# Performance work log

Hardware: AMD Instinct MI355X
Metric: run time of the kernel (lower is better)

Reference implementation:

```python
import jax, jax.numpy as jnp
import numpy as np
from jax import lax

A_RATIOS = (0.5, 1.0, 2.0)
A_SCALES = (8, 16, 32)
FEAT_STRIDE = 16
BASE_SIZE = 16
PRE_NMS = 6000     # n_test_pre_nms
POST_NMS = 300     # n_test_post_nms
NMS_THRESH = 0.7
MIN_SIZE = 16.0
SCALE = 1.0        # forward(scale=1.0) default
NEG = -1e10


def _anchor_base():
    # standard generate_anchor_base: centered at (8,8), ratios x scales
    py = px = BASE_SIZE / 2.0
    rows = []
    for r in A_RATIOS:
        for s in A_SCALES:
            h = BASE_SIZE * s * np.sqrt(r)
            w = BASE_SIZE * s * np.sqrt(1.0 / r)
            rows.append([py - h / 2.0, px - w / 2.0, py + h / 2.0, px + w / 2.0])
    return np.asarray(rows, np.float32)  # (A, 4)


def _all_anchors(height, width):
    base = jnp.asarray(_anchor_base())                                  # (A, 4)
    sy = (jnp.arange(height) * FEAT_STRIDE).astype(jnp.float32)
    sx = (jnp.arange(width) * FEAT_STRIDE).astype(jnp.float32)
    gy, gx = jnp.meshgrid(sy, sx, indexing='ij')
    shift = jnp.stack([gy.ravel(), gx.ravel(), gy.ravel(), gx.ravel()], axis=1)  # (K, 4)
    anch = base[None, :, :] + shift[:, None, :]                         # (K, A, 4)
    return anch.reshape(-1, 4)                                          # (K*A, 4)


def _conv(x, w, b, pad):
    y = lax.conv_general_dilated(x, w, (1, 1), [(pad, pad), (pad, pad)],
                                 dimension_numbers=('NCHW', 'OIHW', 'NCHW'))
    return y + b[None, :, None, None]


def _loc2bbox(anchors, locs):
    h = anchors[:, 2] - anchors[:, 0]
    w = anchors[:, 3] - anchors[:, 1]
    cy = anchors[:, 0] + 0.5 * h
    cx = anchors[:, 1] + 0.5 * w
    dy, dx, dh, dw = locs[:, 0], locs[:, 1], locs[:, 2], locs[:, 3]
    ncy = dy * h + cy
    ncx = dx * w + cx
    nh = jnp.exp(dh) * h
    nw = jnp.exp(dw) * w
    return jnp.stack([ncy - 0.5 * nh, ncx - 0.5 * nw,
                      ncy + 0.5 * nh, ncx + 0.5 * nw], axis=1)


def _iou_one_vs_all(box, boxes):
    ty = jnp.maximum(box[0], boxes[:, 0])
    tx = jnp.maximum(box[1], boxes[:, 1])
    by = jnp.minimum(box[2], boxes[:, 2])
    bx = jnp.minimum(box[3], boxes[:, 3])
    inter = jnp.maximum(by - ty, 0.0) * jnp.maximum(bx - tx, 0.0)
    a1 = (box[2] - box[0]) * (box[3] - box[1])
    a2 = (boxes[:, 2] - boxes[:, 0]) * (boxes[:, 3] - boxes[:, 1])
    return inter / (a1 + a2 - inter + 1e-9)


def _nms(boxes, scores):
    # greedy NMS with fixed POST_NMS output; invalid slots are zero boxes
    def step(s, _):
        i = jnp.argmax(s)
        valid = s[i] > NEG / 2
        ious = _iou_one_vs_all(boxes[i], boxes)
        s = jnp.where(ious > NMS_THRESH, NEG, s)  # suppresses self (iou=1)
        return s, (i, valid)
    _, (idx, valid) = lax.scan(step, scores, None, length=POST_NMS)
    return boxes[idx] * valid[:, None].astype(boxes.dtype)  # (POST_NMS, 4)


def _proposals(anchors, locs, fg, img_h, img_w):
    boxes = _loc2bbox(anchors, locs)
    boxes = jnp.stack([jnp.clip(boxes[:, 0], 0.0, img_h),
                       jnp.clip(boxes[:, 1], 0.0, img_w),
                       jnp.clip(boxes[:, 2], 0.0, img_h),
                       jnp.clip(boxes[:, 3], 0.0, img_w)], axis=1)
    hs = boxes[:, 2] - boxes[:, 0]
    ws = boxes[:, 3] - boxes[:, 1]
    ok = (hs >= MIN_SIZE * SCALE) & (ws >= MIN_SIZE * SCALE)
    sc = jnp.where(ok, fg, NEG)
    top_sc, idx = lax.top_k(sc, PRE_NMS)
    return _nms(boxes[idx], top_sc)


def reference(base_feat, W_conv1, b_conv1, W_score, b_score, W_loc, b_loc, img_h, img_w):
    N, _, H, W = base_feat.shape
    A = 9
    mid = jax.nn.relu(_conv(base_feat, W_conv1, b_conv1, 1))            # (N,512,H,W)
    rpn_locs = _conv(mid, W_loc, b_loc, 0).transpose(0, 2, 3, 1).reshape(N, H * W * A, 4)
    raw = _conv(mid, W_score, b_score, 0).transpose(0, 2, 3, 1)          # (N,H,W,2A)
    rpn_scores = raw.reshape(N, H * W * A, 2)
    fg = jax.nn.softmax(raw.reshape(N, H, W, A, 2), axis=-1)[..., 1].reshape(N, -1)
    anchors = _all_anchors(H, W)                                         # (H*W*A,4)
    ih, iw = float(img_h), float(img_w)
    prop = jax.vmap(lambda l, f: _proposals(anchors, l, f, ih, iw))(rpn_locs, fg)
    rois = prop.reshape(N * POST_NMS, 4)
    roi_indices = jnp.repeat(jnp.arange(N, dtype=jnp.int32), POST_NMS)
    return rpn_locs, rpn_scores, rois, roi_indices, anchors


def setup_inputs() -> dict:
    key = jax.random.key(0)
    k0, k1, k2, k3 = jax.random.split(key, 4)
    N, C, H, W = 4, 512, 64, 64
    nA = 9
    return {
        'base_feat': jax.random.normal(k0, (N, C, H, W), jnp.float32),
        'W_conv1': 0.01 * jax.random.normal(k1, (512, 512, 3, 3), jnp.float32),
        'b_conv1': jnp.zeros((512,), jnp.float32),
        'W_score': 0.01 * jax.random.normal(k2, (2 * nA, 512, 1, 1), jnp.float32),
        'b_score': jnp.zeros((2 * nA,), jnp.float32),
        'W_loc': 0.01 * jax.random.normal(k3, (4 * nA, 512, 1, 1), jnp.float32),
        'b_loc': jnp.zeros((4 * nA,), jnp.float32),
        'img_h': 1024,
        'img_w': 1024,
    }
```

## Files before the change

kernel.cpp:

```cpp
#include <hip/hip_runtime.h>
#include <math.h>

#define HH 64
#define WW 64
#define NIMG 4
#define CIN 512
#define AA 9
#define HWA (HH*WW*AA)
#define PRE_NMS 6000
#define POST_NMS 300
#define NEGV (-1e10f)
#define NEGK 0xD01502F9u
#define NWORD 94

#define OFF1 589824
#define OFF2 884736
#define OFF3 889536
#define OFF4 890736

typedef unsigned int u32;
typedef unsigned long long u64;
typedef _Float16 f16;
typedef _Float16 half8 __attribute__((ext_vector_type(8)));
typedef float f32x4 __attribute__((ext_vector_type(4)));

__device__ __forceinline__ void gload_lds16(const void* g, void* l)
{
    __builtin_amdgcn_global_load_lds((const __attribute__((address_space(1))) void*)g,
                                     (__attribute__((address_space(3))) void*)l,
                                     16, 0, 0);
}

__global__ __launch_bounds__(256) void k_prep_x(const float* __restrict__ x,
                                                f16* __restrict__ xh,
                                                f16* __restrict__ xl)
{
    __shared__ float tile[64][65];
    int ci0 = blockIdx.x * 64, y = blockIdx.y, n = blockIdx.z;
    int t = threadIdx.x;
    #pragma unroll
    for (int l = 0; l < 16; ++l) {
        int idx = l * 256 + t;
        int cc = idx >> 6, xc = idx & 63;
        tile[cc][xc] = x[((size_t)(n * CIN + ci0 + cc) * HH + y) * WW + xc];
    }
    __syncthreads();
    #pragma unroll
    for (int l = 0; l < 16; ++l) {
        int idx = l * 256 + t;
        int xc = idx >> 6, cc = idx & 63;
        float v = tile[cc][xc];
        f16 hi = (f16)v;
        f16 lo = (f16)(v - (float)hi);
        size_t o = ((size_t)(n * 64 + y) * 64 + xc) * 512 + ci0 + cc;
        xh[o] = hi; xl[o] = lo;
    }
}

__global__ __launch_bounds__(256) void k_prep_w(const float* __restrict__ W1,
                                                f16* __restrict__ wh,
                                                f16* __restrict__ wl)
{
    int idx = blockIdx.x * 256 + threadIdx.x;
    int co = idx >> 9, ci = idx & 511;
    #pragma unroll
    for (int tap = 0; tap < 9; ++tap) {
        float v = W1[(size_t)idx * 9 + tap];
        f16 hi = (f16)v;
        f16 lo = (f16)(v - (float)hi);
        size_t o = ((size_t)tap * 512 + co) * 512 + ci;
        wh[o] = hi; wl[o] = lo;
    }
}

__global__ __launch_bounds__(256, 4) void k_conv_mfma(const f16* __restrict__ xh,
                                                      const f16* __restrict__ xl,
                                                      const f16* __restrict__ wh,
                                                      const f16* __restrict__ wl,
                                                      const float* __restrict__ bias,
                                                      float* __restrict__ mid)
{
    __shared__ f16 sX[2][4][64][32];
    const int t = threadIdx.x;
    const int yb = blockIdx.x, co0 = blockIdx.y * 64, n = blockIdx.z;
    const int y0 = yb * 2;
    const int wv = t >> 6, lane = t & 63;
    const int q = lane >> 4, li = lane & 15;
    const int mh = wv & 1;
    const int xhp = wv >> 1;

    if (yb == 0 || yb == 31) {
        int rowu = (yb == 0) ? 0 : 3072;
        u32* p = (u32*)&sX[0][0][0][0];
        #pragma unroll
        for (int l = 0; l < 8; ++l) {
            int idx = l * 256 + t;
            int plane = idx >> 10, r = idx & 1023;
            p[plane * 4096 + rowu + r] = 0;
        }
    }

    f32x4 acc[2][2][2];
    #pragma unroll
    for (int mt = 0; mt < 2; ++mt)
        #pragma unroll
        for (int xn = 0; xn < 2; ++xn)
            #pragma unroll
            for (int yy = 0; yy < 2; ++yy)
                acc[mt][xn][yy] = (f32x4){0.f, 0.f, 0.f, 0.f};

    auto prefetch = [&](int ci0) {
        #pragma unroll
        for (int m = 0; m < 8; ++m) {
            int k2 = wv * 8 + m;
            int plane = k2 >> 4;
            int row = (k2 >> 2) & 3;
            int gy = y0 - 1 + row;
            if ((unsigned)gy < 64u) {
                int col = ((k2 & 3) << 4) + (lane >> 2);
                int s = lane & 3;
                const f16* src = (plane ? xl : xh) +
                    (((size_t)(n * 64 + gy) * 64 + col) * 512 + ci0 + s * 8);
                f16* dst = &sX[0][0][0][0] + (size_t)k2 * 512 + lane * 8;
                gload_lds16(src, dst);
            }
        }
    };

    half8 wa[2][2], wn[2][2];
    auto loadW = [&](half8 w[2][2], int ci0, int tap) {
        #pragma unroll
        for (int mt = 0; mt < 2; ++mt) {
            size_t base = ((size_t)(tap * 512) + co0 + mh * 32 + mt * 16 + li) * 512 + ci0 + q * 8;
            w[0][mt] = *(const half8*)(wh + base);
            w[1][mt] = *(const half8*)(wl + base);
        }
    };

    prefetch(0);
    loadW(wa, 0, 0);

    const half8 zero8 = {(f16)0, (f16)0, (f16)0, (f16)0, (f16)0, (f16)0, (f16)0, (f16)0};

    for (int chunk = 0; chunk < 16; ++chunk) {
        const int ci0 = chunk * 32;
        __syncthreads();

        #pragma unroll
        for (int tap = 0; tap < 9; ++tap) {
            if (tap < 8) loadW(wn, ci0, tap + 1);
            const int ky = tap / 3, kx = tap - ky * 3;

            half8 B[2][2][2];
            #pragma unroll
            for (int xn = 0; xn < 2; ++xn) {
                int xc = xhp * 32 + xn * 16 + li;
                int colr = xc + kx - 1;
                bool oob = (colr < 0) || (colr > 63);
                int colc = oob ? 0 : colr;
                #pragma unroll
                for (int yy = 0; yy < 2; ++yy) {
                    int row = yy + ky;
                    const f16* ph = &sX[0][row][colc][q * 8];
                    half8 vh = *(const half8*)ph;
                    half8 vl = *(const half8*)(ph + 8192);
                    if (oob) { vh = zero8; vl = zero8; }
                    B[0][xn][yy] = vh; B[1][xn][yy] = vl;
                }
            }
            #pragma unroll
            for (int mt = 0; mt < 2; ++mt)
                #pragma unroll
                for (int xn = 0; xn < 2; ++xn)
                    #pragma unroll
                    for (int yy = 0; yy < 2; ++yy)
                        acc[mt][xn][yy] = __builtin_amdgcn_mfma_f32_16x16x32_f16(wa[0][mt], B[0][xn][yy], acc[mt][xn][yy], 0, 0, 0);
            #pragma unroll
            for (int mt = 0; mt < 2; ++mt)
                #pragma unroll
                for (int xn = 0; xn < 2; ++xn)
                    #pragma unroll
                    for (int yy = 0; yy < 2; ++yy)
                        acc[mt][xn][yy] = __builtin_amdgcn_mfma_f32_16x16x32_f16(wa[0][mt], B[1][xn][yy], acc[mt][xn][yy], 0, 0, 0);
            #pragma unroll
            for (int mt = 0; mt < 2; ++mt)
                #pragma unroll
                for (int xn = 0; xn < 2; ++xn)
                    #pragma unroll
                    for (int yy = 0; yy < 2; ++yy)
                        acc[mt][xn][yy] = __builtin_amdgcn_mfma_f32_16x16x32_f16(wa[1][mt], B[0][xn][yy], acc[mt][xn][yy], 0, 0, 0);

            if (tap < 8) {
                #pragma unroll
                for (int pl = 0; pl < 2; ++pl)
                    #pragma unroll
                    for (int mt = 0; mt < 2; ++mt) wa[pl][mt] = wn[pl][mt];
            }
        }

        if (chunk + 1 < 16) {
            __syncthreads();
            prefetch(ci0 + 32);
            loadW(wa, ci0 + 32, 0);
        }
    }

    #pragma unroll
    for (int mt = 0; mt < 2; ++mt) {
        #pragma unroll
        for (int r = 0; r < 4; ++r) {
            int co = co0 + mh * 32 + mt * 16 + q * 4 + r;
            float bv = bias[co];
            #pragma unroll
            for (int xn = 0; xn < 2; ++xn) {
                int xc = xhp * 32 + xn * 16 + li;
                #pragma unroll
                for (int yy = 0; yy < 2; ++yy) {
                    float v = acc[mt][xn][yy][r] + bv;
                    mid[((size_t)(n * 512 + co) * HH + y0 + yy) * WW + xc] = v > 0.f ? v : 0.f;
                }
            }
        }
    }
}

__global__ __launch_bounds__(256) void k_htrans(const float* __restrict__ Ws,
                                                const float* __restrict__ Wl,
                                                float* __restrict__ Wt2)
{
    int i = blockIdx.x * 256 + threadIdx.x;
    if (i >= 512 * 64) return;
    int ci = i >> 6, co = i & 63;
    float v = 0.f;
    if (co < 18) v = Ws[co * 512 + ci];
    else if (co < 54) v = Wl[(co - 18) * 512 + ci];
    Wt2[i] = v;
}

__global__ __launch_bounds__(256) void k_hgemm(const float* __restrict__ mid,
                                               const float* __restrict__ Wt2,
                                               float* __restrict__ sraw)
{
    __shared__ float sM[32][64];
    __shared__ float sW2[32][64];
    const int t = threadIdx.x;
    const int px0 = blockIdx.x * 64, n = blockIdx.y;
    const int tx = t & 15, ty = t >> 4;

    float acc[4][4];
    #pragma unroll
    for (int c = 0; c < 4; ++c)
        #pragma unroll
        for (int j = 0; j < 4; ++j) acc[c][j] = 0.f;

    for (int ci0 = 0; ci0 < 512; ci0 += 32) {
        __syncthreads();
        #pragma unroll
        for (int l = 0; l < 8; ++l) {
            int i = l * 256 + t;
            int ci = i >> 6, px = i & 63;
            sM[ci][px] = mid[((size_t)n * 512 + ci0 + ci) * 4096 + px0 + px];
            sW2[ci][px] = Wt2[(size_t)(ci0 + ci) * 64 + px];
        }
        __syncthreads();
        #pragma unroll
        for (int ci = 0; ci < 32; ++ci) {
            float mv[4], wv[4];
            #pragma unroll
            for (int j = 0; j < 4; ++j) mv[j] = sM[ci][tx * 4 + j];
            #pragma unroll
            for (int c = 0; c < 4; ++c) wv[c] = sW2[ci][ty * 4 + c];
            #pragma unroll
            for (int c = 0; c < 4; ++c)
                #pragma unroll
                for (int j = 0; j < 4; ++j) acc[c][j] += wv[c] * mv[j];
        }
    }
    #pragma unroll
    for (int c = 0; c < 4; ++c) {
        float4 v = make_float4(acc[c][0], acc[c][1], acc[c][2], acc[c][3]);
        *(float4*)&sraw[((size_t)n * 64 + ty * 4 + c) * 4096 + px0 + tx * 4] = v;
    }
}

__global__ __launch_bounds__(256) void k_decode(const float* __restrict__ sraw,
                                                const float* __restrict__ bsc,
                                                const float* __restrict__ blc,
                                                const int* __restrict__ ph,
                                                const int* __restrict__ pw,
                                                float* __restrict__ out,
                                                float* __restrict__ boxes,
                                                u32* __restrict__ key)
{
    int p = blockIdx.x * 256 + threadIdx.x;
    int n = p >> 12, pi = p & 4095;
    int y = pi >> 6, xq = pi & 63;

    if (p < 4800) out[OFF2 + p] = 0.f;
    if (p < 1200) out[OFF3 + p] = (float)(p / 300);

    const float* S = sraw + (size_t)n * 64 * 4096 + pi;
    float* o0 = out + (size_t)n * 147456;
    float* o1 = out + OFF1 + (size_t)n * 73728;
    float IHf = (float)(*ph), IWf = (float)(*pw);

    #pragma unroll
    for (int a = 0; a < 9; ++a) {
        float s0 = S[(size_t)(2 * a) * 4096] + bsc[2 * a];
        float s1 = S[(size_t)(2 * a + 1) * 4096] + bsc[2 * a + 1];
        float dy = S[(size_t)(18 + 4 * a) * 4096] + blc[4 * a];
        float dx = S[(size_t)(19 + 4 * a) * 4096] + blc[4 * a + 1];
        float dh = S[(size_t)(20 + 4 * a) * 4096] + blc[4 * a + 2];
        float dw = S[(size_t)(21 + 4 * a) * 4096] + blc[4 * a + 3];

        o1[(pi * 9 + a) * 2 + 0] = s0;
        o1[(pi * 9 + a) * 2 + 1] = s1;
        o0[(pi * 9 + a) * 4 + 0] = dy;
        o0[(pi * 9 + a) * 4 + 1] = dx;
        o0[(pi * 9 + a) * 4 + 2] = dh;
        o0[(pi * 9 + a) * 4 + 3] = dw;

        float mm = fmaxf(s0, s1);
        float e0 = expf(s0 - mm), e1 = expf(s1 - mm);
        float fg = e1 / (e0 + e1);

        int ri = a / 3, si = a - ri * 3;
        double s = (double)(8 << si);
        double rr = (ri == 0) ? 0.5 : ((ri == 1) ? 1.0 : 2.0);
        double hh = 16.0 * s * sqrt(rr);
        double wd = 16.0 * s * sqrt(1.0 / rr);
        float a0 = (float)(8.0 - hh * 0.5) + (float)(y * 16);
        float a1 = (float)(8.0 - wd * 0.5) + (float)(xq * 16);
        float a2 = (float)(8.0 + hh * 0.5) + (float)(y * 16);
        float a3 = (float)(8.0 + wd * 0.5) + (float)(xq * 16);

        if (n == 0) {
            int ai = pi * 9 + a;
            out[OFF4 + ai * 4 + 0] = a0;
            out[OFF4 + ai * 4 + 1] = a1;
            out[OFF4 + ai * 4 + 2] = a2;
            out[OFF4 + ai * 4 + 3] = a3;
        }

        float h = a2 - a0, w = a3 - a1;
        float cy = a0 + 0.5f * h, cx = a1 + 0.5f * w;
        float ncy = dy * h + cy, ncx = dx * w + cx;
        float nh = expf(dh) * h, nw = expf(dw) * w;
        float b0 = fminf(fmaxf(ncy - 0.5f * nh, 0.f), IHf);
        float b1 = fminf(fmaxf(ncx - 0.5f * nw, 0.f), IWf);
        float b2 = fminf(fmaxf(ncy + 0.5f * nh, 0.f), IHf);
        float b3 = fminf(fmaxf(ncx + 0.5f * nw, 0.f), IWf);

        bool ok = (b2 - b0 >= 16.0f) && (b3 - b1 >= 16.0f);
        float sc = ok ? fg : NEGV;

        int gi = n * HWA + pi * 9 + a;
        ((float4*)boxes)[gi] = make_float4(b0, b1, b2, b3);
        u32 u = __float_as_uint(sc);
        u32 kasc = (u & 0x80000000u) ? ~u : (u | 0x80000000u);
        key[gi] = ~kasc;
    }
}

__global__ __launch_bounds__(1024) void k_select(const u32* __restrict__ key,
                                                 u64* __restrict__ cmp,
                                                 int* __restrict__ nvalid)
{
    __shared__ int hist[256];
    __shared__ u32 sPref;
    __shared__ int sR;
    __shared__ int cLess, cEq, cVal;
    int n = blockIdx.x, t = threadIdx.x;
    const u32* k0 = key + (size_t)n * HWA;

    u32 pref = 0, mask = 0;
    int R = PRE_NMS;
    for (int pass = 0; pass < 4; ++pass) {
        int shift = 24 - pass * 8;
        if (t < 256) hist[t] = 0;
        __syncthreads();
        for (int i = t; i < HWA; i += 1024) {
            u32 k = k0[i];
            if ((k & mask) == pref) atomicAdd(&hist[(k >> shift) & 255], 1);
        }
        __syncthreads();
        if (t == 0) {
            int cum = 0;
            for (int b = 0; b < 256; ++b) {
                int c = hist[b];
                if (cum + c >= R) { sPref = pref | ((u32)b << shift); sR = R - cum; break; }
                cum += c;
            }
        }
        __syncthreads();
        pref = sPref; R = sR; mask |= (0xFFu << shift);
        __syncthreads();
    }
    u32 T = pref;
    if (t == 0) { cLess = 0; cEq = 0; cVal = 0; }
    __syncthreads();
    for (int i = t; i < HWA; i += 1024) {
        u32 k = k0[i];
        if (k < NEGK) atomicAdd(&cVal, 1);
        if (k < T) {
            int p = atomicAdd(&cLess, 1);
            cmp[(size_t)n * 8192 + p] = ((u64)k << 32) | (u32)i;
        } else if (k == T) {
            int p = atomicAdd(&cEq, 1);
            if (p < R) cmp[(size_t)n * 8192 + (PRE_NMS - 1 - p)] = ((u64)k << 32) | (u32)i;
        }
    }
    __syncthreads();
    if (t == 0) nvalid[n] = cVal < PRE_NMS ? cVal : PRE_NMS;
}

__global__ __launch_bounds__(256) void k_rank2(const u64* __restrict__ cmp,
                                               const float* __restrict__ boxes,
                                               float* __restrict__ boxesS)
{
    __shared__ u64 sK[PRE_NMS];
    int n = blockIdx.y;
    int t = threadIdx.x;
    const u64* K = cmp + (size_t)n * 8192;
    for (int j = t; j < PRE_NMS; j += 256) sK[j] = K[j];
    __syncthreads();
    int i = blockIdx.x * 256 + t;
    if (i >= PRE_NMS) return;
    u64 ki = sK[i];
    int rank = 0;
    #pragma unroll 8
    for (int j = 0; j < PRE_NMS; ++j)
        rank += (sK[j] < ki) ? 1 : 0;
    u32 idx = (u32)(ki & 0xFFFFFFFFu);
    ((float4*)boxesS)[(size_t)n * PRE_NMS + rank] =
        ((const float4*)boxes)[(size_t)n * HWA + idx];
}

__global__ __launch_bounds__(256) void k_iou(const float* __restrict__ boxesS,
                                             u64* __restrict__ mask)
{
    __shared__ float4 cb[256];
    int wg = blockIdx.x, ic = blockIdx.y, n = blockIdx.z;
    if (wg * 4 + 3 < ic) return;
    int t = threadIdx.x;
    const float4* B = (const float4*)boxesS + (size_t)n * PRE_NMS;
    int jc = wg * 256 + t;
    cb[t] = (jc < PRE_NMS) ? B[jc] : make_float4(0.f, 0.f, 0.f, 0.f);
    __syncthreads();
    int ws = t >> 6;
    int w = wg * 4 + ws;
    int i = ic * 64 + (t & 63);
    if (i >= PRE_NMS || w >= NWORD) return;
    float4 bb = B[i];
    float area1 = (bb.z - bb.x) * (bb.w - bb.y);
    u64 m = 0;
    #pragma unroll 8
    for (int j = 0; j < 64; ++j) {
        float4 o = cb[ws * 64 + j];
        float ty_ = fmaxf(bb.x, o.x), tx_ = fmaxf(bb.y, o.y);
        float by_ = fminf(bb.z, o.z), bx_ = fminf(bb.w, o.w);
        float inter = fmaxf(by_ - ty_, 0.f) * fmaxf(bx_ - tx_, 0.f);
        float area2 = (o.z - o.x) * (o.w - o.y);
        float iou = inter / (area1 + area2 - inter + 1e-9f);
        if (iou > 0.7f) m |= (1ull << j);
    }
    mask[((size_t)n * PRE_NMS + i) * NWORD + w] = m;
}

__global__ __launch_bounds__(64) void k_nms4(const u64* __restrict__ mask,
                                             const int* __restrict__ nvalid,
                                             const float* __restrict__ boxesS,
                                             float* __restrict__ rois)
{
    int n = blockIdx.x, lane = threadIdx.x;
    int nv = nvalid[n];
    const u64* M = mask + (size_t)n * PRE_NMS * NWORD;
    const float4* B = (const float4*)boxesS + (size_t)n * PRE_NMS;

    auto vmask = [&](int w) -> u64 {
        int lo = w * 64;
        if (nv >= lo + 64) return ~0ull;
        if (nv <= lo) return 0ull;
        return (1ull << (nv - lo)) - 1ull;
    };
    u64 vm0 = vmask(lane);
    u64 vm1 = (lane < NWORD - 64) ? vmask(64 + lane) : 0ull;
    u64 rem0 = 0, rem1 = 0;

    int cnt = 0;
    while (cnt < POST_NMS) {
        u64 t0 = (~rem0) & vm0;
        u64 t1 = (~rem1) & vm1;
        int cand[8];
        int nc = 0;
        #pragma unroll
        for (int k = 0; k < 8; ++k) {
            u64 b0 = __ballot(t0 != 0);
            int c = -1;
            if (b0) {
                int l = __builtin_ctzll(b0);
                u64 w = __shfl(t0, l);
                c = l * 64 + __builtin_ctzll(w);
                if (lane == l) t0 &= t0 - 1;
            } else {
                u64 b1 = __ballot(t1 != 0);
                if (b1) {
                    int l = __builtin_ctzll(b1);
                    u64 w = __shfl(t1, l);
                    c = (64 + l) * 64 + __builtin_ctzll(w);
                    if (lane == l) t1 &= t1 - 1;
                }
            }
            if (c < 0) break;
            cand[nc++] = c;
        }
        if (nc == 0) break;

        u64 r0[8], r1[8];
        for (int k = 0; k < nc; ++k) {
            const u64* Mr = M + (size_t)cand[k] * NWORD;
            r0[k] = Mr[lane];
            r1[k] = (lane < NWORD - 64) ? Mr[64 + lane] : 0ull;
        }

        for (int k = 0; k < nc && cnt < POST_NMS; ++k) {
            int c = cand[k];
            int w = c >> 6, b = c & 63;
            u64 cw = (w < 64) ? __shfl(rem0, w) : __shfl(rem1, w - 64);
            if (!((cw >> b) & 1ull)) {
                if (lane == 0) {
                    float4 bb = B[c];
                    float* orow = rois + (size_t)(n * POST_NMS + cnt) * 4;
                    orow[0] = bb.x; orow[1] = bb.y; orow[2] = bb.z; orow[3] = bb.w;
                }
                rem0 |= r0[k];
                rem1 |= r1[k];
                cnt++;
            }
        }
    }
}

extern "C" void kernel_launch(void* const* d_in, const int* in_sizes, int n_in,
                              void* d_out, int out_size, void* d_ws, size_t ws_size,
                              hipStream_t stream)
{
    const float* x  = (const float*)d_in[0];
    const float* W1 = (const float*)d_in[1];
    const float* b1 = (const float*)d_in[2];
    const float* Ws = (const float*)d_in[3];
    const float* bs = (const float*)d_in[4];
    const float* Wl = (const float*)d_in[5];
    const float* bl = (const float*)d_in[6];
    const int* ih   = (const int*)d_in[7];
    const int* iw   = (const int*)d_in[8];
    float* out = (float*)d_out;
    char* ws = (char*)d_ws;

    f16*   Wh2    = (f16*)  (ws);
    f16*   Wl2    = (f16*)  (ws + 4718592);
    float* mid    = (float*)(ws + 9437184);
    f16*   xh     = (f16*)  (ws + 42991616);
    f16*   xl     = (f16*)  (ws + 59768832);
    float* boxes  = (float*)(ws + 42991616);
    u32*   key    = (u32*)  (ws + 45350912);
    u64*   cmp    = (u64*)  (ws + 45940736);
    float* boxesS = (float*)(ws + 46202880);
    int*   nval   = (int*)  (ws + 46586880);
    float* Wt2    = (float*)(ws);
    float* sraw   = (float*)(ws + 262144);
    u64*   iomask = (u64*)  (ws + 9437184);

    k_prep_x<<<dim3(8, 64, 4), 256, 0, stream>>>(x, xh, xl);
    k_prep_w<<<1024, 256, 0, stream>>>(W1, Wh2, Wl2);
    k_conv_mfma<<<dim3(32, 8, 4), 256, 0, stream>>>(xh, xl, Wh2, Wl2, b1, mid);
    k_htrans<<<128, 256, 0, stream>>>(Ws, Wl, Wt2);
    k_hgemm<<<dim3(64, 4), 256, 0, stream>>>(mid, Wt2, sraw);
    k_decode<<<64, 256, 0, stream>>>(sraw, bs, bl, ih, iw, out, boxes, key);
    k_select<<<4, 1024, 0, stream>>>(key, cmp, nval);
    k_rank2<<<dim3(24, NIMG), 256, 0, stream>>>(cmp, boxes, boxesS);
    k_iou<<<dim3(24, NWORD, NIMG), 256, 0, stream>>>(boxesS, iomask);
    k_nms4<<<NIMG, 64, 0, stream>>>(iomask, nval, boxesS, out + OFF2);
}
```

Baseline: 919.5 us.

## Use 32x32x16 MFMA in conv and warp-aggregate atomics in top-k select

New measurement: 963.7 us. +4.8%, slower.

```diff
diff --git a/kernel.cpp b/kernel.cpp
--- a/kernel.cpp
+++ b/kernel.cpp
@@ -22,7 +22,7 @@
 typedef unsigned long long u64;
 typedef _Float16 f16;
 typedef _Float16 half8 __attribute__((ext_vector_type(8)));
-typedef float f32x4 __attribute__((ext_vector_type(4)));
+typedef float f32x16 __attribute__((ext_vector_type(16)));
 
 __device__ __forceinline__ void gload_lds16(const void* g, void* l)
 {
@@ -85,7 +85,7 @@
     const int yb = blockIdx.x, co0 = blockIdx.y * 64, n = blockIdx.z;
     const int y0 = yb * 2;
     const int wv = t >> 6, lane = t & 63;
-    const int q = lane >> 4, li = lane & 15;
+    const int ln31 = lane & 31, lh = lane >> 5;
     const int mh = wv & 1;
     const int xhp = wv >> 1;
 
@@ -100,14 +100,11 @@
         }
     }
 
-    f32x4 acc[2][2][2];
-    #pragma unroll
-    for (int mt = 0; mt < 2; ++mt)
-        #pragma unroll
-        for (int xn = 0; xn < 2; ++xn)
-            #pragma unroll
-            for (int yy = 0; yy < 2; ++yy)
-                acc[mt][xn][yy] = (f32x4){0.f, 0.f, 0.f, 0.f};
+    f32x16 acc[2];
+    #pragma unroll
+    for (int yy = 0; yy < 2; ++yy)
+        #pragma unroll
+        for (int r = 0; r < 16; ++r) acc[yy][r] = 0.f;
 
     auto prefetch = [&](int ci0) {
         #pragma unroll
@@ -130,10 +127,10 @@
     half8 wa[2][2], wn[2][2];
     auto loadW = [&](half8 w[2][2], int ci0, int tap) {
         #pragma unroll
-        for (int mt = 0; mt < 2; ++mt) {
-            size_t base = ((size_t)(tap * 512) + co0 + mh * 32 + mt * 16 + li) * 512 + ci0 + q * 8;
-            w[0][mt] = *(const half8*)(wh + base);
-            w[1][mt] = *(const half8*)(wl + base);
+        for (int ks = 0; ks < 2; ++ks) {
+            size_t base = ((size_t)(tap * 512) + co0 + mh * 32 + ln31) * 512 + ci0 + ks * 16 + lh * 8;
+            w[0][ks] = *(const half8*)(wh + base);
+            w[1][ks] = *(const half8*)(wl + base);
         }
     };
 
@@ -151,50 +148,43 @@
             if (tap < 8) loadW(wn, ci0, tap + 1);
             const int ky = tap / 3, kx = tap - ky * 3;
 
+            int xc = xhp * 32 + ln31;
+            int colr = xc + kx - 1;
+            bool oob = (colr < 0) || (colr > 63);
+            int colc = oob ? 0 : colr;
             half8 B[2][2][2];
             #pragma unroll
-            for (int xn = 0; xn < 2; ++xn) {
-                int xc = xhp * 32 + xn * 16 + li;
-                int colr = xc + kx - 1;
-                bool oob = (colr < 0) || (colr > 63);
-                int colc = oob ? 0 : colr;
+            for (int ks = 0; ks < 2; ++ks) {
                 #pragma unroll
                 for (int yy = 0; yy < 2; ++yy) {
-                    int row = yy + ky;
-                    const f16* ph = &sX[0][row][colc][q * 8];
+                    const f16* ph = &sX[0][yy + ky][colc][ks * 16 + lh * 8];
                     half8 vh = *(const half8*)ph;
                     half8 vl = *(const half8*)(ph + 8192);
                     if (oob) { vh = zero8; vl = zero8; }
-                    B[0][xn][yy] = vh; B[1][xn][yy] = vl;
+                    B[0][ks][yy] = vh; B[1][ks][yy] = vl;
                 }
             }
             #pragma unroll
-            for (int mt = 0; mt < 2; ++mt)
+            for (int ks = 0; ks < 2; ++ks)
                 #pragma unroll
-                for (int xn = 0; xn < 2; ++xn)
-                    #pragma unroll
-                    for (int yy = 0; yy < 2; ++yy)
-                        acc[mt][xn][yy] = __builtin_amdgcn_mfma_f32_16x16x32_f16(wa[0][mt], B[0][xn][yy], acc[mt][xn][yy], 0, 0, 0);
-            #pragma unroll
-            for (int mt = 0; mt < 2; ++mt)
+                for (int yy = 0; yy < 2; ++yy)
+                    acc[yy] = __builtin_amdgcn_mfma_f32_32x32x16_f16(wa[0][ks], B[0][ks][yy], acc[yy], 0, 0, 0);
+            #pragma unroll
+            for (int ks = 0; ks < 2; ++ks)
                 #pragma unroll
-                for (int xn = 0; xn < 2; ++xn)
-                    #pragma unroll
-                    for (int yy = 0; yy < 2; ++yy)
-                        acc[mt][xn][yy] = __builtin_amdgcn_mfma_f32_16x16x32_f16(wa[0][mt], B[1][xn][yy], acc[mt][xn][yy], 0, 0, 0);
-            #pragma unroll
-            for (int mt = 0; mt < 2; ++mt)
+                for (int yy = 0; yy < 2; ++yy)
+                    acc[yy] = __builtin_amdgcn_mfma_f32_32x32x16_f16(wa[0][ks], B[1][ks][yy], acc[yy], 0, 0, 0);
+            #pragma unroll
+            for (int ks = 0; ks < 2; ++ks)
                 #pragma unroll
-                for (int xn = 0; xn < 2; ++xn)
-                    #pragma unroll
-                    for (int yy = 0; yy < 2; ++yy)
-                        acc[mt][xn][yy] = __builtin_amdgcn_mfma_f32_16x16x32_f16(wa[1][mt], B[0][xn][yy], acc[mt][xn][yy], 0, 0, 0);
+                for (int yy = 0; yy < 2; ++yy)
+                    acc[yy] = __builtin_amdgcn_mfma_f32_32x32x16_f16(wa[1][ks], B[0][ks][yy], acc[yy], 0, 0, 0);
 
             if (tap < 8) {
                 #pragma unroll
                 for (int pl = 0; pl < 2; ++pl)
                     #pragma unroll
-                    for (int mt = 0; mt < 2; ++mt) wa[pl][mt] = wn[pl][mt];
+                    for (int ks = 0; ks < 2; ++ks) wa[pl][ks] = wn[pl][ks];
             }
         }
 
@@ -206,20 +196,13 @@
     }
 
     #pragma unroll
-    for (int mt = 0; mt < 2; ++mt) {
-        #pragma unroll
-        for (int r = 0; r < 4; ++r) {
-            int co = co0 + mh * 32 + mt * 16 + q * 4 + r;
-            float bv = bias[co];
-            #pragma unroll
-            for (int xn = 0; xn < 2; ++xn) {
-                int xc = xhp * 32 + xn * 16 + li;
-                #pragma unroll
-                for (int yy = 0; yy < 2; ++yy) {
-                    float v = acc[mt][xn][yy][r] + bv;
-                    mid[((size_t)(n * 512 + co) * HH + y0 + yy) * WW + xc] = v > 0.f ? v : 0.f;
-                }
-            }
+    for (int yy = 0; yy < 2; ++yy) {
+        #pragma unroll
+        for (int r = 0; r < 16; ++r) {
+            int co = co0 + mh * 32 + (r & 3) + 8 * (r >> 2) + 4 * lh;
+            int xc = xhp * 32 + ln31;
+            float v = acc[yy][r] + bias[co];
+            mid[((size_t)(n * 512 + co) * HH + y0 + yy) * WW + xc] = v > 0.f ? v : 0.f;
         }
     }
 }
@@ -370,7 +353,7 @@
     __shared__ u32 sPref;
     __shared__ int sR;
     __shared__ int cLess, cEq, cVal;
-    int n = blockIdx.x, t = threadIdx.x;
+    int n = blockIdx.x, t = threadIdx.x, lane = t & 63;
     const u32* k0 = key + (size_t)n * HWA;
 
     u32 pref = 0, mask = 0;
@@ -381,7 +364,16 @@
         __syncthreads();
         for (int i = t; i < HWA; i += 1024) {
             u32 k = k0[i];
-            if ((k & mask) == pref) atomicAdd(&hist[(k >> shift) & 255], 1);
+            bool act = ((k & mask) == pref);
+            u32 bin = (k >> shift) & 255;
+            u64 active = __ballot(act);
+            while (active) {
+                int leader = __builtin_ctzll(active);
+                u32 lbin = __shfl(bin, leader);
+                u64 same = __ballot(act && (bin == lbin));
+                if (lane == leader) atomicAdd(&hist[lbin], (int)__popcll(same));
+                active &= ~same;
+            }
         }
         __syncthreads();
         if (t == 0) {
@@ -401,13 +393,29 @@
     __syncthreads();
     for (int i = t; i < HWA; i += 1024) {
         u32 k = k0[i];
-        if (k < NEGK) atomicAdd(&cVal, 1);
-        if (k < T) {
-            int p = atomicAdd(&cLess, 1);
-            cmp[(size_t)n * 8192 + p] = ((u64)k << 32) | (u32)i;
-        } else if (k == T) {
-            int p = atomicAdd(&cEq, 1);
-            if (p < R) cmp[(size_t)n * 8192 + (PRE_NMS - 1 - p)] = ((u64)k << 32) | (u32)i;
+        u64 vmv = __ballot(k < NEGK);
+        if (vmv && lane == 0) atomicAdd(&cVal, (int)__popcll(vmv));
+        u64 lm = __ballot(k < T);
+        if (lm) {
+            int ldr = __builtin_ctzll(lm);
+            int base = 0;
+            if (lane == ldr) base = atomicAdd(&cLess, (int)__popcll(lm));
+            base = __shfl(base, ldr);
+            if (k < T) {
+                int p = base + (int)__popcll(lm & ((1ull << lane) - 1ull));
+                cmp[(size_t)n * 8192 + p] = ((u64)k << 32) | (u32)i;
+            }
+        }
+        u64 em = __ballot(k == T);
+        if (em) {
+            int ldr = __builtin_ctzll(em);
+            int base = 0;
+            if (lane == ldr) base = atomicAdd(&cEq, (int)__popcll(em));
+            base = __shfl(base, ldr);
+            if (k == T) {
+                int p = base + (int)__popcll(em & ((1ull << lane) - 1ull));
+                if (p < R) cmp[(size_t)n * 8192 + (PRE_NMS - 1 - p)] = ((u64)k << 32) | (u32)i;
+            }
         }
     }
     __syncthreads();
```
